# Kernel optimization log

Measured on AMD Instinct MI355X. Metric: run time of the kernel, lower is better.

Reference implementation:

```python
import jax, jax.numpy as jnp
import numpy as np

EPS = 1e-5

def _bn(x, g, b, m, v):
    # inference-mode BatchNorm2d over channel dim of NCHW
    inv = jax.lax.rsqrt(v + EPS)
    return (x - m[None, :, None, None]) * (g * inv)[None, :, None, None] + b[None, :, None, None]

def _conv1x1(x, w, b):
    # x: [B,C,H,W], w: [O,C], b: [O]
    return jnp.einsum('bchw,oc->bohw', x, w) + b[None, :, None, None]

def setup_inputs() -> dict:
    key = jax.random.key(0)
    ks = jax.random.split(key, 20)
    B, C, H, W = 16, 512, 64, 64
    C2, C4 = C // 2, C // 4
    d = {}
    d['x'] = jax.random.normal(ks[0], (B, C, H, W), jnp.float32)
    # query_conv_p1: Conv2d(512->256, k1) + BN + ReLU
    d['q1_w'] = jax.random.normal(ks[1], (C2, C), jnp.float32) * (1.0 / np.sqrt(C))
    d['q1_b'] = jax.random.normal(ks[2], (C2,), jnp.float32) * 0.01
    d['bn1_g'] = jax.random.uniform(ks[3], (C2,), jnp.float32, 0.5, 1.5)
    d['bn1_b'] = jax.random.normal(ks[4], (C2,), jnp.float32) * 0.01
    d['bn1_m'] = jax.random.normal(ks[5], (C2,), jnp.float32) * 0.01
    d['bn1_v'] = jax.random.uniform(ks[6], (C2,), jnp.float32, 0.5, 1.5)
    # query_conv_p2: Conv2d(256->128, k1) + BN + ReLU
    d['q2_w'] = jax.random.normal(ks[7], (C4, C2), jnp.float32) * (1.0 / np.sqrt(C2))
    d['q2_b'] = jax.random.normal(ks[8], (C4,), jnp.float32) * 0.01
    d['bn2_g'] = jax.random.uniform(ks[9], (C4,), jnp.float32, 0.5, 1.5)
    d['bn2_b'] = jax.random.normal(ks[10], (C4,), jnp.float32) * 0.01
    d['bn2_m'] = jax.random.normal(ks[11], (C4,), jnp.float32) * 0.01
    d['bn2_v'] = jax.random.uniform(ks[12], (C4,), jnp.float32, 0.5, 1.5)
    # py1_prop: Conv1d(256->256, k1)  (py2_prop is never used in forward)
    d['p1_w'] = jax.random.normal(ks[13], (C2, C2), jnp.float32) * (1.0 / np.sqrt(C2))
    d['p1_b'] = jax.random.normal(ks[14], (C2,), jnp.float32) * 0.01
    # fusion_conv: Conv2d(512->512, k3, pad 1) + BN + ReLU
    d['fus_w'] = jax.random.normal(ks[15], (C, C, 3, 3), jnp.float32) * (1.0 / np.sqrt(C * 9))
    d['fus_b'] = jax.random.normal(ks[16], (C,), jnp.float32) * 0.01
    d['bn3_g'] = jax.random.uniform(ks[17], (C,), jnp.float32, 0.5, 1.5)
    d['bn3_b'] = jax.random.normal(ks[18], (C,), jnp.float32) * 0.01
    d['bn3_m'] = jnp.zeros((C,), jnp.float32)
    d['bn3_v'] = jnp.ones((C,), jnp.float32)
    # gamma: torch init is zeros(1); use small random so the attention branch is live
    d['gamma'] = jax.random.normal(ks[19], (1,), jnp.float32) * 0.1
    return d

def reference(x, q1_w, q1_b, bn1_g, bn1_b, bn1_m, bn1_v,
              q2_w, q2_b, bn2_g, bn2_b, bn2_m, bn2_v,
              p1_w, p1_b, fus_w, fus_b, bn3_g, bn3_b, bn3_m, bn3_v, gamma):
    B, C, H, W = x.shape
    C2, C4 = C // 2, C // 4
    py1 = jax.nn.relu(_bn(_conv1x1(x, q1_w, q1_b), bn1_g, bn1_b, bn1_m, bn1_v))   # [B,256,H,W]
    py2 = jax.nn.relu(_bn(_conv1x1(py1, q2_w, q2_b), bn2_g, bn2_b, bn2_m, bn2_v))  # [B,128,H,W]
    pq1 = py1.reshape(B, C2, -1)   # [B,256,HW]
    pk1 = x.reshape(B, C, -1)      # [B,512,HW]
    # energy_py1 = pq1 @ pk1^T -> [B,256,512]; Conv1d(k1) over channel dim; permute -> [B,512,256]
    e1 = jnp.einsum('bcn,bdn->bcd', pq1, pk1)
    e1 = jnp.einsum('oc,bcd->bod', p1_w, e1) + p1_b[None, :, None]
    e1 = e1.transpose(0, 2, 1)     # [B,512,256]
    pq2 = py2.reshape(B, C4, -1)   # [B,128,HW]
    # energy_py2 = (pq2 @ py1^T).permute -> [B,256,128]; same py1_prop conv applied
    e2 = jnp.einsum('bcn,bdn->bcd', pq2, py1.reshape(B, C2, -1)).transpose(0, 2, 1)  # [B,256,128]
    e2 = jnp.einsum('oc,bcd->bod', p1_w, e2) + p1_b[None, :, None]                    # [B,256,128]
    energy = jnp.einsum('bce,bed->bcd', e1, e2)  # [B,512,128]
    energy_new = jnp.max(energy, axis=-1, keepdims=True) - energy
    attention = jax.nn.softmax(energy_new, axis=-1)  # [B,512,128]
    out = jnp.einsum('bcd,bdn->bcn', attention, pq2)  # [B,512,HW]
    out = out.reshape(B, C, H, W)
    out = gamma[0] * out + x
    out = jax.lax.conv_general_dilated(out, fus_w, window_strides=(1, 1),
                                       padding=((1, 1), (1, 1)),
                                       dimension_numbers=('NCHW', 'OIHW', 'NCHW'))
    out = out + fus_b[None, :, None, None]
    out = jax.nn.relu(_bn(out, bn3_g, bn3_b, bn3_m, bn3_v))
    return out
```

## Files before the change

### kernel.cpp

```cpp
#include <hip/hip_runtime.h>
#include <math.h>

#define BATCH 16
#define CH    512
#define CH2   256
#define CH4   128
#define HH    64
#define WW    64
#define HWSZ  4096
#define EPSV  1e-5f
#define HP 66
#define WP 66

typedef _Float16 f16x8 __attribute__((ext_vector_type(8)));
typedef float    f32x4 __attribute__((ext_vector_type(4)));

#define GLOBAL_AS __attribute__((address_space(1)))
#define LDS_AS    __attribute__((address_space(3)))

__device__ __forceinline__ void gload16(const void* g, void* l) {
    __builtin_amdgcn_global_load_lds((const GLOBAL_AS unsigned int*)g,
                                     (LDS_AS unsigned int*)l, 16, 0, 0);
}

__device__ __forceinline__ ushort f2h(float v) {
    _Float16 h = (_Float16)v;
    return *(ushort*)&h;
}
__device__ __forceinline__ float h2f(ushort u) {
    _Float16 h = *(_Float16*)&u;
    return (float)h;
}

__global__ void prep_params(
    const float* __restrict__ q1_b, const float* __restrict__ g1, const float* __restrict__ b1,
    const float* __restrict__ m1, const float* __restrict__ v1,
    const float* __restrict__ q2_b, const float* __restrict__ g2, const float* __restrict__ b2,
    const float* __restrict__ m2, const float* __restrict__ v2,
    const float* __restrict__ fus_b, const float* __restrict__ g3, const float* __restrict__ b3,
    const float* __restrict__ m3, const float* __restrict__ v3,
    float* __restrict__ s1, float* __restrict__ t1,
    float* __restrict__ s2, float* __restrict__ t2,
    float* __restrict__ s3, float* __restrict__ t3)
{
    int i = threadIdx.x;
    if (i < CH2) { float s = g1[i] * rsqrtf(v1[i] + EPSV); s1[i] = s; t1[i] = (q1_b[i] - m1[i]) * s + b1[i]; }
    if (i < CH4) { float s = g2[i] * rsqrtf(v2[i] + EPSV); s2[i] = s; t2[i] = (q2_b[i] - m2[i]) * s + b2[i]; }
    if (i < CH)  { float s = g3[i] * rsqrtf(v3[i] + EPSV); s3[i] = s; t3[i] = (fus_b[i] - m3[i]) * s + b3[i]; }
}

__global__ void transpose_p1(const float* __restrict__ p1w, float* __restrict__ p1T)
{
    int c = blockIdx.x;
    int o = threadIdx.x;
    p1T[c * CH2 + o] = p1w[o * CH2 + c];
}

__global__ void repack_w(const float* __restrict__ fw, ushort* __restrict__ wH)
{
    int o = blockIdx.x;
    int c = threadIdx.x;
    const float* src = fw + ((size_t)o * CH + c) * 9;
    #pragma unroll
    for (int t = 0; t < 9; ++t)
        wH[((size_t)t * CH + o) * CH + c] = f2h(src[t]);
}

__global__ void cvt_h(const float* __restrict__ s, ushort* __restrict__ d, int n)
{
    int i = blockIdx.x * blockDim.x + threadIdx.x;
    if (i < n) d[i] = f2h(s[i]);
}

__global__ void zero_border(ushort* __restrict__ preH)
{
    int i = blockIdx.x * blockDim.x + threadIdx.x;
    const int q  = i & 63;
    const int px = (i >> 6) % 260;
    const int b  = i / (260 * 64);
    int hp, wp;
    if (px < 66)       { hp = 0;            wp = px; }
    else if (px < 132) { hp = 65;           wp = px - 66; }
    else if (px < 196) { hp = px - 132 + 1; wp = 0; }
    else               { hp = px - 196 + 1; wp = 65; }
    const uint4 z = make_uint4(0u, 0u, 0u, 0u);
    *(uint4*)&preH[((size_t)(b * HP + hp) * WP + wp) * CH + q * 8] = z;
}

__global__ __launch_bounds__(256)
void cvt_x(const float* __restrict__ x, ushort* __restrict__ xHc, ushort* __restrict__ xHp)
{
    __shared__ float t[64][68];
    const int b  = blockIdx.z;
    const int c0 = blockIdx.y * 64;
    const int p0 = blockIdx.x * 64;
    const int tid = threadIdx.x;
    const int tx = tid & 15, ty = tid >> 4;

    const float* xb = x + ((size_t)b * CH + c0) * HWSZ + p0;
    #pragma unroll
    for (int it = 0; it < 4; ++it) {
        const int r = ty + it * 16;
        float4 v = *(const float4*)&xb[(size_t)r * HWSZ + tx * 4];
        *(float4*)&t[r][tx * 4] = v;
        ushort4 u = make_ushort4(f2h(v.x), f2h(v.y), f2h(v.z), f2h(v.w));
        *(ushort4*)&xHc[((size_t)b * CH + c0 + r) * HWSZ + p0 + tx * 4] = u;
    }
    __syncthreads();
    #pragma unroll
    for (int it = 0; it < 4; ++it) {
        const int p = ty + it * 16;
        const int c = tx * 4;
        ushort4 u = make_ushort4(f2h(t[c + 0][p]), f2h(t[c + 1][p]),
                                 f2h(t[c + 2][p]), f2h(t[c + 3][p]));
        *(ushort4*)&xHp[((size_t)b * HWSZ + p0 + p) * CH + c0 + c] = u;
    }
}

template<int EPI>
__global__ __launch_bounds__(256)
void hgemm(const ushort* __restrict__ A, const ushort* __restrict__ B,
           void* __restrict__ C0, void* __restrict__ C1,
           int N, int KP, int ldA, int ldB, int ldHp,
           long sA, long sB, long sC0, long sC1, long pStride,
           const float* __restrict__ scale, const float* __restrict__ shift,
           const ushort* __restrict__ XHp, const float* __restrict__ gamma)
{
    __shared__ alignas(16) ushort As[4096];
    __shared__ alignas(16) ushort Bs[4096];

    const int b  = blockIdx.z & 15;
    const int pk = blockIdx.z >> 4;
    const int m0 = blockIdx.y * 128;
    const int n0 = blockIdx.x * 128;
    const int kBase = pk * KP;

    const int tid  = threadIdx.x;
    const int lane = tid & 63;
    const int wv   = tid >> 6;
    const int wm   = wv >> 1;
    const int wn   = wv & 1;

    const int cpart = (lane & 3) * 8;
    const int prow  = lane >> 2;
    const int rA0 = wv * 32 + prow;
    const int rA1 = rA0 + 16;

    const ushort* Ag = A + (size_t)b * sA;
    const ushort* Bg = B + (size_t)b * sB;
    const ushort* aSrc0 = Ag + (size_t)(m0 + rA0) * ldA + cpart + kBase;
    const ushort* aSrc1 = Ag + (size_t)(m0 + rA1) * ldA + cpart + kBase;
    const ushort* bSrc0 = Bg + (size_t)(n0 + rA0) * ldB + cpart + kBase;
    const ushort* bSrc1 = Bg + (size_t)(n0 + rA1) * ldB + cpart + kBase;
    ushort* AsW = &As[wv * 1024];
    ushort* BsW = &Bs[wv * 1024];

    const int fr = lane & 15, fg = lane >> 4;
    const int aOff = (wm * 64 + fr) * 32 + fg * 8;
    const int bOff = (wn * 64 + fr) * 32 + fg * 8;

    f32x4 acc[4][4];
    const f32x4 vzero = {0.f, 0.f, 0.f, 0.f};
    #pragma unroll
    for (int i = 0; i < 4; ++i)
        #pragma unroll
        for (int j = 0; j < 4; ++j) acc[i][j] = vzero;

    for (int k0 = 0; k0 < KP; k0 += 32) {
        gload16(aSrc0 + k0, AsW);
        gload16(aSrc1 + k0, AsW + 512);
        gload16(bSrc0 + k0, BsW);
        gload16(bSrc1 + k0, BsW + 512);
        __syncthreads();

        f16x8 aF[4], bF[4];
        #pragma unroll
        for (int mi = 0; mi < 4; ++mi) aF[mi] = *(const f16x8*)&As[aOff + mi * 512];
        #pragma unroll
        for (int ni = 0; ni < 4; ++ni) bF[ni] = *(const f16x8*)&Bs[bOff + ni * 512];
        #pragma unroll
        for (int mi = 0; mi < 4; ++mi)
            #pragma unroll
            for (int ni = 0; ni < 4; ++ni)
                acc[mi][ni] = __builtin_amdgcn_mfma_f32_16x16x32_f16(aF[mi], bF[ni], acc[mi][ni], 0, 0, 0);
        __syncthreads();
    }

    #pragma unroll
    for (int mi = 0; mi < 4; ++mi) {
        const int mBase = m0 + wm * 64 + mi * 16 + fg * 4;
        #pragma unroll
        for (int ni = 0; ni < 4; ++ni) {
            const int n = n0 + wn * 64 + ni * 16 + fr;
            if constexpr (EPI == 0) {
                ushort us[4];
                #pragma unroll
                for (int reg = 0; reg < 4; ++reg) {
                    const int m = mBase + reg;
                    float v = fmaxf(acc[mi][ni][reg] * scale[m] + shift[m], 0.0f);
                    us[reg] = f2h(v);
                    ((ushort*)C0)[(size_t)b * sC0 + (size_t)m * N + n] = us[reg];
                }
                *(ushort4*)&((ushort*)C1)[(size_t)b * sC1 + (size_t)n * ldHp + mBase] =
                    make_ushort4(us[0], us[1], us[2], us[3]);
            }
            if constexpr (EPI == 1) {
                float* C = (float*)C0 + pk * pStride + (size_t)b * sC0;
                #pragma unroll
                for (int reg = 0; reg < 4; ++reg)
                    C[(size_t)(mBase + reg) * N + n] = acc[mi][ni][reg];
            }
            if constexpr (EPI == 2) {
                const int h = n >> 6, w = n & 63;
                const float g = gamma[0];
                ushort4 xv = *(const ushort4*)&XHp[((size_t)b * HWSZ + n) * CH + mBase];
                ushort4 pk4;
                pk4.x = f2h(g * acc[mi][ni][0] + h2f(xv.x));
                pk4.y = f2h(g * acc[mi][ni][1] + h2f(xv.y));
                pk4.z = f2h(g * acc[mi][ni][2] + h2f(xv.z));
                pk4.w = f2h(g * acc[mi][ni][3] + h2f(xv.w));
                *(ushort4*)&((ushort*)C0)[((size_t)(b * HP + h + 1) * WP + (w + 1)) * CH + mBase] = pk4;
            }
        }
    }
}

__global__ void reduce_parts(float* __restrict__ dst, const float* __restrict__ src,
                             int n4, int parts, long pstride)
{
    for (int i = blockIdx.x * blockDim.x + threadIdx.x; i < n4; i += gridDim.x * blockDim.x) {
        float4 s = ((const float4*)src)[i];
        for (int p = 1; p < parts; ++p) {
            const float4 v = *(const float4*)&src[(size_t)p * pstride + (size_t)i * 4];
            s.x += v.x; s.y += v.y; s.z += v.z; s.w += v.w;
        }
        ((float4*)dst)[i] = s;
    }
}

template<int EPI>
__global__ __launch_bounds__(256)
void gemm_ab(const float* __restrict__ A, const float* __restrict__ Bm,
             float* __restrict__ Cm,
             int M, int N, int K,
             long sA, long sB, long sC,
             const float* __restrict__ shift)
{
    __shared__ float As[16][68];
    __shared__ float Bs[16][68];

    const int b   = blockIdx.z;
    const float* Ab = A  + (long)b * sA;
    const float* Bb = Bm + (long)b * sB;

    const int m0 = blockIdx.y * 64;
    const int n0 = blockIdx.x * 64;
    const int tid = threadIdx.x;
    const int tx = tid & 15;
    const int ty = tid >> 4;

    const int a_m = tid >> 2;
    const int a_k = (tid & 3) * 4;
    const int b_k = tid >> 4;
    const int b_n = (tid & 15) * 4;

    float acc[4][4] = {};

    for (int k0 = 0; k0 < K; k0 += 16) {
        float4 av = *(const float4*)&Ab[(long)(m0 + a_m) * K + k0 + a_k];
        float4 bv = *(const float4*)&Bb[(long)(k0 + b_k) * N + n0 + b_n];
        As[a_k + 0][a_m] = av.x;
        As[a_k + 1][a_m] = av.y;
        As[a_k + 2][a_m] = av.z;
        As[a_k + 3][a_m] = av.w;
        *(float4*)&Bs[b_k][b_n] = bv;
        __syncthreads();
        #pragma unroll
        for (int k = 0; k < 16; ++k) {
            float4 a4 = *(const float4*)&As[k][ty * 4];
            float4 b4 = *(const float4*)&Bs[k][tx * 4];
            float ar[4] = {a4.x, a4.y, a4.z, a4.w};
            float br[4] = {b4.x, b4.y, b4.z, b4.w};
            #pragma unroll
            for (int i = 0; i < 4; ++i)
                #pragma unroll
                for (int j = 0; j < 4; ++j)
                    acc[i][j] += ar[i] * br[j];
        }
        __syncthreads();
    }

    float* Cb = Cm + (long)b * sC;
    #pragma unroll
    for (int i = 0; i < 4; ++i) {
        const int m = m0 + ty * 4 + i;
        float v[4];
        #pragma unroll
        for (int j = 0; j < 4; ++j) {
            float val = acc[i][j];
            if constexpr (EPI == 2) { val = val + shift[n0 + tx * 4 + j]; }
            v[j] = val;
        }
        *(float4*)&Cb[(long)m * N + n0 + tx * 4] = make_float4(v[0], v[1], v[2], v[3]);
    }
}

__global__ __launch_bounds__(256)
void gemm_abT(const float* __restrict__ A, const float* __restrict__ Bm,
              float* __restrict__ Cm,
              int M, int N, int K,
              long sA, long sB, long sC,
              const float* __restrict__ shift)
{
    __shared__ float As[16][68];
    __shared__ float Bs[16][68];

    const int b   = blockIdx.z;
    const float* Ab = A  + (long)b * sA;
    const float* Bb = Bm + (long)b * sB;
    float*       Cb = Cm + (long)b * sC;

    const int m0 = blockIdx.y * 64;
    const int n0 = blockIdx.x * 64;
    const int tid = threadIdx.x;
    const int tx = tid & 15;
    const int ty = tid >> 4;

    const int r  = tid >> 2;
    const int kq = (tid & 3) * 4;

    float acc[4][4] = {};

    for (int k0 = 0; k0 < K; k0 += 16) {
        float4 av = *(const float4*)&Ab[(long)(m0 + r) * K + k0 + kq];
        float4 bv = *(const float4*)&Bb[(long)(n0 + r) * K + k0 + kq];
        As[kq + 0][r] = av.x; As[kq + 1][r] = av.y; As[kq + 2][r] = av.z; As[kq + 3][r] = av.w;
        Bs[kq + 0][r] = bv.x; Bs[kq + 1][r] = bv.y; Bs[kq + 2][r] = bv.z; Bs[kq + 3][r] = bv.w;
        __syncthreads();
        #pragma unroll
        for (int k = 0; k < 16; ++k) {
            float4 a4 = *(const float4*)&As[k][ty * 4];
            float4 b4 = *(const float4*)&Bs[k][tx * 4];
            float ar[4] = {a4.x, a4.y, a4.z, a4.w};
            float br[4] = {b4.x, b4.y, b4.z, b4.w};
            #pragma unroll
            for (int i = 0; i < 4; ++i)
                #pragma unroll
                for (int j = 0; j < 4; ++j)
                    acc[i][j] += ar[i] * br[j];
        }
        __syncthreads();
    }

    #pragma unroll
    for (int i = 0; i < 4; ++i) {
        const int m = m0 + ty * 4 + i;
        float v[4];
        #pragma unroll
        for (int j = 0; j < 4; ++j) v[j] = acc[i][j] + shift[m];
        *(float4*)&Cb[(long)m * N + n0 + tx * 4] = make_float4(v[0], v[1], v[2], v[3]);
    }
}

__global__ void softmax_rows(const float* __restrict__ e, ushort* __restrict__ attH)
{
    const int row  = blockIdx.x;
    const int lane = threadIdx.x;
    const float* p = e + (long)row * CH4;
    float a = p[lane];
    float c = p[lane + 64];
    float mn = fminf(a, c);
    #pragma unroll
    for (int off = 32; off; off >>= 1) mn = fminf(mn, __shfl_xor(mn, off));
    float ea = expf(mn - a);
    float ec = expf(mn - c);
    float s = ea + ec;
    #pragma unroll
    for (int off = 32; off; off >>= 1) s += __shfl_xor(s, off);
    float inv = 1.0f / s;
    attH[(long)row * CH4 + lane]      = f2h(ea * inv);
    attH[(long)row * CH4 + lane + 64] = f2h(ec * inv);
}

__global__ __launch_bounds__(256)
void conv3_direct(const ushort* __restrict__ preH, const ushort* __restrict__ wH,
                  const float* __restrict__ s3, const float* __restrict__ t3,
                  float* __restrict__ outp)
{
    __shared__ alignas(16) ushort Pt[4 * 66 * 32];
    __shared__ alignas(16) ushort Wl[128 * 32];

    const int bid = blockIdx.x;
    const int lin = (bid & 7) * 256 + (bid >> 3);
    const int ob  = lin >> 9;
    const int pt  = lin & 511;
    const int b   = pt >> 5;
    const int h0  = (pt & 31) * 2;
    const int o0  = ob * 128;

    const int tid  = threadIdx.x;
    const int lane = tid & 63;
    const int wv   = tid >> 6;
    const int wm   = wv >> 1;
    const int wn   = wv & 1;

    const int cpart = (lane & 3) * 8;
    const int prow  = lane >> 2;

    const size_t aBase0 = (size_t)(o0 + wv * 32 + prow) * CH + cpart;
    const size_t aBase1 = aBase0 + (size_t)16 * CH;
    ushort* WlW = &Wl[wv * 1024];

    const size_t pRow0 = ((size_t)(b * HP + h0) * WP + 1) * CH;
    const size_t pLane = (size_t)(wv * 16 + prow) * CH + cpart;

    const int fr = lane & 15, fg = lane >> 4;
    const int aOff = (wm * 64 + fr) * 32 + fg * 8;
    const int bLaneOff = (wn * 66 + fr) * 32 + fg * 8;

    f32x4 acc[4][4];
    const f32x4 vzero = {0.f, 0.f, 0.f, 0.f};
    #pragma unroll
    for (int i = 0; i < 4; ++i)
        #pragma unroll
        for (int j = 0; j < 4; ++j) acc[i][j] = vzero;

    for (int c0 = 0; c0 < CH; c0 += 32) {
        #pragma unroll
        for (int rp = 0; rp < 4; ++rp)
            gload16(preH + pRow0 + (size_t)rp * WP * CH + pLane + c0,
                    &Pt[(rp * 66 + 1 + wv * 16) * 32]);
        if (tid < 32) {
            const int e  = tid >> 4;
            const int rr = (tid >> 2) & 3;
            const int q  = tid & 3;
            const uint4 v = *(const uint4*)&preH[((size_t)(b * HP + h0 + rr) * WP + e * 65) * CH + c0 + q * 8];
            *(uint4*)&Pt[(rr * 66 + e * 65) * 32 + q * 8] = v;
        }

        #pragma unroll
        for (int t = 0; t < 9; ++t) {
            const int r = t / 3, s = t - (t / 3) * 3;
            gload16(wH + (size_t)t * CH * CH + aBase0 + c0, WlW);
            gload16(wH + (size_t)t * CH * CH + aBase1 + c0, WlW + 512);
            __syncthreads();

            f16x8 aF[4], bF[4];
            #pragma unroll
            for (int mi = 0; mi < 4; ++mi) aF[mi] = *(const f16x8*)&Wl[aOff + mi * 512];
            #pragma unroll
            for (int ni = 0; ni < 4; ++ni)
                bF[ni] = *(const f16x8*)&Pt[bLaneOff + (r * 66 + s + ni * 16) * 32];
            #pragma unroll
            for (int mi = 0; mi < 4; ++mi)
                #pragma unroll
                for (int ni = 0; ni < 4; ++ni)
                    acc[mi][ni] = __builtin_amdgcn_mfma_f32_16x16x32_f16(aF[mi], bF[ni], acc[mi][ni], 0, 0, 0);
            __syncthreads();
        }
    }

    #pragma unroll
    for (int mi = 0; mi < 4; ++mi) {
        #pragma unroll
        for (int reg = 0; reg < 4; ++reg) {
            const int o = o0 + wm * 64 + mi * 16 + fg * 4 + reg;
            const float sc = s3[o], tt = t3[o];
            #pragma unroll
            for (int ni = 0; ni < 4; ++ni) {
                const int pix = wn * 64 + ni * 16 + fr;
                const float val = fmaxf(acc[mi][ni][reg] * sc + tt, 0.0f);
                outp[(size_t)(b * CH + o) * HWSZ + (h0 + (pix >> 6)) * WW + (pix & 63)] = val;
            }
        }
    }
}

extern "C" void kernel_launch(void* const* d_in, const int* in_sizes, int n_in,
                              void* d_out, int out_size, void* d_ws, size_t ws_size,
                              hipStream_t stream)
{
    const float* x     = (const float*)d_in[0];
    const float* q1_w  = (const float*)d_in[1];
    const float* q1_b  = (const float*)d_in[2];
    const float* bn1_g = (const float*)d_in[3];
    const float* bn1_b = (const float*)d_in[4];
    const float* bn1_m = (const float*)d_in[5];
    const float* bn1_v = (const float*)d_in[6];
    const float* q2_w  = (const float*)d_in[7];
    const float* q2_b  = (const float*)d_in[8];
    const float* bn2_g = (const float*)d_in[9];
    const float* bn2_b = (const float*)d_in[10];
    const float* bn2_m = (const float*)d_in[11];
    const float* bn2_v = (const float*)d_in[12];
    const float* p1_w  = (const float*)d_in[13];
    const float* p1_b  = (const float*)d_in[14];
    const float* fus_w = (const float*)d_in[15];
    const float* fus_b = (const float*)d_in[16];
    const float* bn3_g = (const float*)d_in[17];
    const float* bn3_b = (const float*)d_in[18];
    const float* bn3_m = (const float*)d_in[19];
    const float* bn3_v = (const float*)d_in[20];
    const float* gamma = (const float*)d_in[21];
    float* outp = (float*)d_out;

    float* ws = (float*)d_ws;
    size_t off = 0;
    ushort* py2Hp = (ushort*)(ws + off); off += (size_t)BATCH * HWSZ * CH4 / 2;
    ushort* attH  = (ushort*)(ws + off); off += (size_t)BATCH * CH * CH4 / 2;
    ushort* wH    = (ushort*)(ws + off); off += (size_t)9 * CH * CH / 2;
    ushort* q1_wH = (ushort*)(ws + off); off += (size_t)CH2 * CH / 2;
    ushort* q2_wH = (ushort*)(ws + off); off += (size_t)CH4 * CH2 / 2;
    float* e1T    = ws + off; off += (size_t)BATCH * CH * CH2;
    float* e2     = ws + off; off += (size_t)BATCH * CH4 * CH2;
    float* e2p    = ws + off; off += (size_t)BATCH * CH2 * CH4;
    float* p1T    = ws + off; off += (size_t)CH2 * CH2;
    float* e1Tparts = ws + off; off += 2 * (size_t)BATCH * CH * CH2;
    float* e1pt   = e1Tparts;
    float* energy = e1Tparts + (size_t)BATCH * CH * CH2;
    ushort* xHp   = (ushort*)(ws + off); off += (size_t)BATCH * HWSZ * CH / 2;
    float* R = ws + off; off += (size_t)5 * BATCH * HWSZ * CH2 / 2;
    ushort* py1Hc = (ushort*)R;
    ushort* py1Hp = py1Hc + (size_t)BATCH * HWSZ * CH2;
    ushort* py2Hc = py1Hp + (size_t)BATCH * HWSZ * CH2;
    ushort* preH  = (ushort*)R;
    float* xHcR = ws + off; off += (size_t)BATCH * HWSZ * CH / 2;
    ushort* xHc    = (ushort*)xHcR;
    float* e2parts = xHcR;
    float* s1 = ws + off; off += CH2;
    float* t1 = ws + off; off += CH2;
    float* s2 = ws + off; off += CH4;
    float* t2 = ws + off; off += CH4;
    float* s3 = ws + off; off += CH;
    float* t3 = ws + off; off += CH;

    const long sXc  = (long)CH  * HWSZ;
    const long sXp  = (long)HWSZ * CH;
    const long sP1c = (long)CH2 * HWSZ;
    const long sP1p = (long)HWSZ * CH2;
    const long sP2c = (long)CH4 * HWSZ;
    const long sP2p = (long)HWSZ * CH4;

    prep_params<<<1, 512, 0, stream>>>(q1_b, bn1_g, bn1_b, bn1_m, bn1_v,
                                       q2_b, bn2_g, bn2_b, bn2_m, bn2_v,
                                       fus_b, bn3_g, bn3_b, bn3_m, bn3_v,
                                       s1, t1, s2, t2, s3, t3);
    transpose_p1<<<CH2, CH2, 0, stream>>>(p1_w, p1T);
    repack_w<<<CH, CH, 0, stream>>>(fus_w, wH);
    cvt_h<<<(CH2 * CH + 255) / 256, 256, 0, stream>>>(q1_w, q1_wH, CH2 * CH);
    cvt_h<<<(CH4 * CH2 + 255) / 256, 256, 0, stream>>>(q2_w, q2_wH, CH4 * CH2);
    cvt_x<<<dim3(64, 8, BATCH), 256, 0, stream>>>(x, xHc, xHp);

    hgemm<0><<<dim3(32, 2, BATCH), 256, 0, stream>>>(
        q1_wH, xHp, py1Hc, py1Hp, HWSZ, CH, CH, CH, CH2,
        0, sXp, sP1c, sP1p, 0, s1, t1, nullptr, nullptr);

    hgemm<0><<<dim3(32, 1, BATCH), 256, 0, stream>>>(
        q2_wH, py1Hp, py2Hc, py2Hp, HWSZ, CH2, CH2, CH2, CH4,
        0, sP1p, sP2c, sP2p, 0, s2, t2, nullptr, nullptr);

    hgemm<1><<<dim3(2, 4, 2 * BATCH), 256, 0, stream>>>(
        xHc, py1Hc, e1Tparts, nullptr, CH2, 2048, HWSZ, HWSZ, 0,
        sXc, sP1c, (long)CH * CH2, 0, (long)BATCH * CH * CH2, nullptr, nullptr, nullptr, nullptr);
    reduce_parts<<<1024, 256, 0, stream>>>(e1T, e1Tparts,
        (int)((size_t)BATCH * CH * CH2 / 4), 2, (long)BATCH * CH * CH2);

    hgemm<1><<<dim3(2, 1, 8 * BATCH), 256, 0, stream>>>(
        py2Hc, py1Hc, e2parts, nullptr, CH2, 512, HWSZ, HWSZ, 0,
        sP2c, sP1c, (long)CH4 * CH2, 0, (long)BATCH * CH4 * CH2, nullptr, nullptr, nullptr, nullptr);
    reduce_parts<<<512, 256, 0, stream>>>(e2, e2parts,
        (int)((size_t)BATCH * CH4 * CH2 / 4), 8, (long)BATCH * CH4 * CH2);

    gemm_abT<<<dim3(2, 4, BATCH), 256, 0, stream>>>(
        p1_w, e2, e2p, CH2, CH4, CH2, 0, (long)CH4 * CH2, (long)CH2 * CH4, p1_b);

    gemm_ab<2><<<dim3(4, 8, BATCH), 256, 0, stream>>>(
        e1T, p1T, e1pt, CH, CH2, CH2, (long)CH * CH2, 0, (long)CH * CH2, p1_b);

    gemm_ab<3><<<dim3(2, 8, BATCH), 256, 0, stream>>>(
        e1pt, e2p, energy, CH, CH4, CH2, (long)CH * CH2, (long)CH2 * CH4, (long)CH * CH4,
        nullptr);

    softmax_rows<<<BATCH * CH, 64, 0, stream>>>(energy, attH);

    zero_border<<<(BATCH * 260 * 64 + 255) / 256, 256, 0, stream>>>(preH);
    hgemm<2><<<dim3(32, 4, BATCH), 256, 0, stream>>>(
        attH, py2Hp, preH, nullptr, HWSZ, CH4, CH4, CH4, 0,
        (long)CH * CH4, sP2p, 0, 0, 0, nullptr, nullptr, xHp, gamma);

    conv3_direct<<<2048, 256, 0, stream>>>(preH, wH, s3, t3, outp);
}
```

Before: 921.0 us.

## Double-buffer conv3 weight tiles and prefetch next tap during MFMA

Rewrites the 3x3 conv kernel so weight tiles for the next tap are loaded into a second LDS buffer while the current tap's MFMAs run, replacing two __syncthreads per tap with explicit waitcnt plus barriers. Border pixels for all channel chunks are preloaded once into LDS instead of read by scalar global loads every chunk. MFMA sections are given higher wave priority. This aims to hide global load latency behind compute, at the cost of more LDS use and delicate hand-written vmcnt accounting.

```diff
diff --git a/kernel.cpp b/kernel.cpp
--- a/kernel.cpp
+++ b/kernel.cpp
@@ -383,12 +383,13 @@
 }
 
 __global__ __launch_bounds__(256)
-void conv3_direct(const ushort* __restrict__ preH, const ushort* __restrict__ wH,
-                  const float* __restrict__ s3, const float* __restrict__ t3,
-                  float* __restrict__ outp)
+void conv3_pipe(const ushort* __restrict__ preH, const ushort* __restrict__ wH,
+                const float* __restrict__ s3, const float* __restrict__ t3,
+                float* __restrict__ outp)
 {
     __shared__ alignas(16) ushort Pt[4 * 66 * 32];
-    __shared__ alignas(16) ushort Wl[128 * 32];
+    __shared__ alignas(16) ushort Wl[2][4096];
+    __shared__ alignas(16) ushort PeAll[8 * 512];
 
     const int bid = blockIdx.x;
     const int lin = (bid & 7) * 256 + (bid >> 3);
@@ -409,7 +410,6 @@
 
     const size_t aBase0 = (size_t)(o0 + wv * 32 + prow) * CH + cpart;
     const size_t aBase1 = aBase0 + (size_t)16 * CH;
-    ushort* WlW = &Wl[wv * 1024];
 
     const size_t pRow0 = ((size_t)(b * HP + h0) * WP + 1) * CH;
     const size_t pLane = (size_t)(wv * 16 + prow) * CH + cpart;
@@ -425,38 +425,73 @@
         #pragma unroll
         for (int j = 0; j < 4; ++j) acc[i][j] = vzero;
 
-    for (int c0 = 0; c0 < CH; c0 += 32) {
-        #pragma unroll
-        for (int rp = 0; rp < 4; ++rp)
-            gload16(preH + pRow0 + (size_t)rp * WP * CH + pLane + c0,
-                    &Pt[(rp * 66 + 1 + wv * 16) * 32]);
-        if (tid < 32) {
-            const int e  = tid >> 4;
-            const int rr = (tid >> 2) & 3;
-            const int q  = tid & 3;
-            const uint4 v = *(const uint4*)&preH[((size_t)(b * HP + h0 + rr) * WP + e * 65) * CH + c0 + q * 8];
-            *(uint4*)&Pt[(rr * 66 + e * 65) * 32 + q * 8] = v;
-        }
-
+    #pragma unroll
+    for (int rp = 0; rp < 4; ++rp)
+        gload16(preH + pRow0 + (size_t)rp * WP * CH + pLane,
+                &Pt[(rp * 66 + 1 + wv * 16) * 32]);
+    #pragma unroll
+    for (int k = 0; k < 2; ++k) {
+        const int reg = wv * 2 + k;
+        const int rr = reg >> 1, e = reg & 1;
+        gload16(preH + ((size_t)(b * HP + h0 + rr) * WP + e * 65) * CH + lane * 8,
+                &PeAll[reg * 512]);
+    }
+    gload16(wH + aBase0, &Wl[0][wv * 1024]);
+    gload16(wH + aBase1, &Wl[0][wv * 1024 + 512]);
+    asm volatile("s_waitcnt vmcnt(0)" ::: "memory");
+    __builtin_amdgcn_s_barrier();
+    if (tid < 32) {
+        const int e = tid >> 4, rr = (tid >> 2) & 3, q = tid & 3;
+        *(uint4*)&Pt[(rr * 66 + e * 65) * 32 + q * 8] =
+            *(const uint4*)&PeAll[(rr * 2 + e) * 512 + q * 8];
+    }
+    asm volatile("s_waitcnt lgkmcnt(0)" ::: "memory");
+    __builtin_amdgcn_s_barrier();
+
+    for (int cc = 0; cc < 16; ++cc) {
+        const int c0 = cc * 32;
         #pragma unroll
         for (int t = 0; t < 9; ++t) {
+            const int wp = (cc + t) & 1;
+            if (t < 8) {
+                gload16(wH + (size_t)(t + 1) * CH * CH + aBase0 + c0, &Wl[wp ^ 1][wv * 1024]);
+                gload16(wH + (size_t)(t + 1) * CH * CH + aBase1 + c0, &Wl[wp ^ 1][wv * 1024 + 512]);
+            } else if (cc < 15) {
+                gload16(wH + aBase0 + c0 + 32, &Wl[wp ^ 1][wv * 1024]);
+                gload16(wH + aBase1 + c0 + 32, &Wl[wp ^ 1][wv * 1024 + 512]);
+            }
+            asm volatile("s_waitcnt vmcnt(2)" ::: "memory");
+            if (t == 0)
+                asm volatile("s_waitcnt lgkmcnt(0)" ::: "memory");
+            __builtin_amdgcn_s_barrier();
+
             const int r = t / 3, s = t - (t / 3) * 3;
-            gload16(wH + (size_t)t * CH * CH + aBase0 + c0, WlW);
-            gload16(wH + (size_t)t * CH * CH + aBase1 + c0, WlW + 512);
-            __syncthreads();
-
             f16x8 aF[4], bF[4];
             #pragma unroll
-            for (int mi = 0; mi < 4; ++mi) aF[mi] = *(const f16x8*)&Wl[aOff + mi * 512];
+            for (int mi = 0; mi < 4; ++mi) aF[mi] = *(const f16x8*)&Wl[wp][aOff + mi * 512];
             #pragma unroll
             for (int ni = 0; ni < 4; ++ni)
                 bF[ni] = *(const f16x8*)&Pt[bLaneOff + (r * 66 + s + ni * 16) * 32];
+            __builtin_amdgcn_s_setprio(1);
             #pragma unroll
             for (int mi = 0; mi < 4; ++mi)
                 #pragma unroll
                 for (int ni = 0; ni < 4; ++ni)
                     acc[mi][ni] = __builtin_amdgcn_mfma_f32_16x16x32_f16(aF[mi], bF[ni], acc[mi][ni], 0, 0, 0);
-            __syncthreads();
+            __builtin_amdgcn_s_setprio(0);
+            __builtin_amdgcn_s_barrier();
+        }
+        if (cc < 15) {
+            const int c0n = c0 + 32;
+            #pragma unroll
+            for (int rp = 0; rp < 4; ++rp)
+                gload16(preH + pRow0 + (size_t)rp * WP * CH + pLane + c0n,
+                        &Pt[(rp * 66 + 1 + wv * 16) * 32]);
+            if (tid < 32) {
+                const int e = tid >> 4, rr = (tid >> 2) & 3, q = tid & 3;
+                *(uint4*)&Pt[(rr * 66 + e * 65) * 32 + q * 8] =
+                    *(const uint4*)&PeAll[(rr * 2 + e) * 512 + c0n + q * 8];
+            }
         }
     }
 
@@ -588,5 +623,5 @@
         attH, py2Hp, preH, nullptr, HWSZ, CH4, CH4, CH4, 0,
         (long)CH * CH4, sP2p, 0, 0, 0, nullptr, nullptr, xHp, gamma);
 
-    conv3_direct<<<2048, 256, 0, stream>>>(preH, wH, s3, t3, outp);
-}
+    conv3_pipe<<<2048, 256, 0, stream>>>(preH, wH, s3, t3, outp);
+}
```

Result: no change. 913.2 us (-0.8%).
